# Kernel optimization log

Hardware: AMD Instinct MI355X
Metric: run time of the kernel (lower is better)

Reference implementation:

```python
import jax, jax.numpy as jnp
import numpy as np

B, N, D, NS, ITERS = 64, 4096, 256, 8, 3
EPS_ATTN = 1e-5   # module eps (added to attn)
EPS_LN = 1e-5     # torch LayerNorm default eps


def layer_norm(x, g, b):
    m = jnp.mean(x, axis=-1, keepdims=True)
    v = jnp.mean((x - m) ** 2, axis=-1, keepdims=True)
    return (x - m) / jnp.sqrt(v + EPS_LN) * g + b


def setup_inputs() -> dict:
    key = jax.random.key(0)
    ks = jax.random.split(key, 16)
    s = 0.02
    return {
        "inputs": jax.random.normal(ks[0], (B, N, D), jnp.float32),
        "slots_init": jax.random.normal(ks[1], (1, NS, D), jnp.float32),
        "Wq": jax.random.normal(ks[2], (D, D), jnp.float32) * s,
        "Wk": jax.random.normal(ks[3], (D, D), jnp.float32) * s,
        "Wv": jax.random.normal(ks[4], (D, D), jnp.float32) * s,
        "W_ih": jax.random.normal(ks[5], (3 * D, D), jnp.float32) * s,
        "W_hh": jax.random.normal(ks[6], (3 * D, D), jnp.float32) * s,
        "b_ih": jnp.zeros((3 * D,), jnp.float32),
        "b_hh": jnp.zeros((3 * D,), jnp.float32),
        "ln_in_g": jnp.ones((D,), jnp.float32),
        "ln_in_b": jnp.zeros((D,), jnp.float32),
        "ln_s_g": jnp.ones((D,), jnp.float32),
        "ln_s_b": jnp.zeros((D,), jnp.float32),
        "ln_m_g": jnp.ones((D,), jnp.float32),
        "ln_m_b": jnp.zeros((D,), jnp.float32),
        "W1": jax.random.normal(ks[7], (4 * D, D), jnp.float32) * s,
        "b1": jnp.zeros((4 * D,), jnp.float32),
        "W2": jax.random.normal(ks[8], (D, 4 * D), jnp.float32) * s,
        "b2": jnp.zeros((D,), jnp.float32),
    }


def gru_cell(x, h, W_ih, W_hh, b_ih, b_hh):
    # x, h: [M, D]; PyTorch GRU cell equations (gate order r, z, n)
    gi = x @ W_ih.T + b_ih
    gh = h @ W_hh.T + b_hh
    gi_r, gi_z, gi_n = jnp.split(gi, 3, axis=-1)
    gh_r, gh_z, gh_n = jnp.split(gh, 3, axis=-1)
    r = jax.nn.sigmoid(gi_r + gh_r)
    z = jax.nn.sigmoid(gi_z + gh_z)
    n = jnp.tanh(gi_n + r * gh_n)
    return (1.0 - z) * n + z * h


def reference(inputs, slots_init, Wq, Wk, Wv, W_ih, W_hh, b_ih, b_hh,
              ln_in_g, ln_in_b, ln_s_g, ln_s_b, ln_m_g, ln_m_b,
              W1, b1, W2, b2):
    b, n, d = inputs.shape
    scale = d ** -0.5
    slots = jnp.broadcast_to(slots_init, (b, NS, d))

    x = layer_norm(inputs, ln_in_g, ln_in_b)
    k = x @ Wk.T  # [b, n, d]
    v = x @ Wv.T  # [b, n, d]

    for _ in range(ITERS):
        slots_prev = slots
        s_n = layer_norm(slots, ln_s_g, ln_s_b)
        q = s_n @ Wq.T  # [b, ns, d]
        dots = jnp.einsum('bid,bjd->bij', q, k) * scale  # [b, ns, n]
        attn = jax.nn.softmax(dots, axis=1) + EPS_ATTN   # softmax over slots
        attn = attn / jnp.mean(attn, axis=-1, keepdims=True)
        updates = jnp.einsum('bjd,bij->bid', v, attn)     # [b, ns, d]
        h = gru_cell(updates.reshape(-1, d), slots_prev.reshape(-1, d),
                     W_ih, W_hh, b_ih, b_hh)
        slots = h.reshape(b, NS, d)
        # residual MLP with pre-norm
        y = layer_norm(slots, ln_m_g, ln_m_b)
        y = jax.nn.leaky_relu(y @ W1.T + b1, negative_slope=0.01)
        slots = slots + (y @ W2.T + b2)
    return slots
```

## Files before the change

### kernel.cpp

```cpp
#include <hip/hip_runtime.h>
#include <hip/hip_fp16.h>
#include <hip/hip_bf16.h>

#define BB 64
#define NN 4096
#define DD 256
#define NSL 8
#define NITER 3

__device__ __forceinline__ float wredsum(float v){
#pragma unroll
  for(int m=32;m;m>>=1) v += __shfl_xor(v, m, 64);
  return v;
}
__device__ __forceinline__ float2 u2f2(unsigned u){ __half2 h; __builtin_memcpy(&h,&u,4); return __half22float2(h); }
__device__ __forceinline__ float sigm(float v){ return 1.0f/(1.0f+__expf(-v)); }

union U4 { uint4 u; __half2 h[4]; };

__device__ __forceinline__ void st8(float* dst, uint4 uu){
  U4 v; v.u=uu;
  float2 f0=__half22float2(v.h[0]), f1=__half22float2(v.h[1]),
         f2=__half22float2(v.h[2]), f3=__half22float2(v.h[3]);
  dst[0]=f0.x; dst[1]=f0.y; dst[2]=f1.x; dst[3]=f1.y;
  dst[4]=f2.x; dst[5]=f2.y; dst[6]=f3.x; dst[7]=f3.y;
}

__global__ __launch_bounds__(256) void kp_all(
    const float* __restrict__ Whh, const float* __restrict__ W1,
    const float* __restrict__ W2,  const float* __restrict__ sinit,
    const float* __restrict__ Wih, const float* __restrict__ Wv,
    const float* __restrict__ Wq,  const float* __restrict__ Wk,
    __half* __restrict__ Wg, __half* __restrict__ W1t, __half* __restrict__ W2t,
    float* __restrict__ slots, __half* __restrict__ M2h, float* __restrict__ zbuf){
  int bid=blockIdx.x, t=threadIdx.x;
  if(bid<1664){
    for(int idx=bid*256+t; idx<851968; idx+=1664*256){
      if(idx<196608){ int col=idx>>8, c=idx&255; Wg[(size_t)c*1536+768+col]=__float2half(Whh[idx]); }
      else if(idx<458752){ int k=idx-196608; int col=k>>8, c=k&255; W1t[(size_t)c*1024+col]=__float2half(W1[k]); }
      else if(idx<720896){ int k=idx-458752; int col=k>>10, c=k&1023; W2t[(size_t)c*256+col]=__float2half(W2[k]); }
      else { int k=idx-720896; slots[k]=sinit[k&2047]; }
    }
  } else if(bid<2432){
    int col=bid-1664;
    __shared__ float wr[256];
    wr[t]=Wih[col*256+t];
    __syncthreads();
    float acc=0.f;
#pragma unroll 8
    for(int d=0;d<256;d++) acc += wr[d]*Wv[d*256+t];
    Wg[(size_t)t*1536+col]=__float2half(acc);
  } else if(bid<2688){
    int c=bid-2432;
    float acc=0.f;
#pragma unroll 8
    for(int d=0;d<256;d++) acc += Wq[d*256+t]*Wk[d*256+c];
    M2h[(size_t)c*256+t]=__float2half(acc*0.0625f);
  } else {
    int idx=(bid-2688)*256+t;
    if(idx<394752) zbuf[idx]=0.f;
  }
}

__global__ __launch_bounds__(256) void k_ln_x(const float* __restrict__ in, const float* __restrict__ g,
                                              const float* __restrict__ bbv, __half* __restrict__ x){
  int row  = blockIdx.x*4 + (threadIdx.x>>6);
  int lane = threadIdx.x&63;
  const float4 v = ((const float4*)(in + (size_t)row*DD))[lane];
  float s  = v.x+v.y+v.z+v.w;
  float ss = v.x*v.x+v.y*v.y+v.z*v.z+v.w*v.w;
  s = wredsum(s); ss = wredsum(ss);
  float m = s*(1.0f/256.0f);
  float r = rsqrtf(ss*(1.0f/256.0f) - m*m + 1e-5f);
  float4 gv = ((const float4*)g)[lane];
  float4 bv = ((const float4*)bbv)[lane];
  float y0=(v.x-m)*r*gv.x+bv.x, y1=(v.y-m)*r*gv.y+bv.y;
  float y2=(v.z-m)*r*gv.z+bv.z, y3=(v.w-m)*r*gv.w+bv.w;
  __half2 h0=__floats2half2_rn(y0,y1), h1=__floats2half2_rn(y2,y3);
  uint2 u; __builtin_memcpy(&u.x,&h0,4); __builtin_memcpy(&u.y,&h1,4);
  ((uint2*)(x + (size_t)row*DD))[lane] = u;
}

__global__ __launch_bounds__(256) void k_pre(const float* __restrict__ slots, const float* __restrict__ g,
                                             const float* __restrict__ bbv, const __half* __restrict__ M2h,
                                             float* __restrict__ qs, __half* __restrict__ slotsh){
  int row = blockIdx.x;
  int t = threadIdx.x;
  __shared__ __align__(16) float sn[256];
  __shared__ float red[8];
  float v = slots[row*256 + t];
  slotsh[(size_t)row*256+t]=__float2half(v);
  float s = wredsum(v), ss = wredsum(v*v);
  int wid=t>>6, lane=t&63;
  if(lane==0){ red[wid]=s; red[4+wid]=ss; }
  __syncthreads();
  float S  = red[0]+red[1]+red[2]+red[3];
  float SS = red[4]+red[5]+red[6]+red[7];
  float m = S*(1.0f/256.0f);
  float r = rsqrtf(SS*(1.0f/256.0f) - m*m + 1e-5f);
  sn[t] = (v-m)*r*g[t]+bbv[t];
  __syncthreads();
  const uint4* w4 = (const uint4*)(M2h + (size_t)t*256);
  float acc=0.f;
#pragma unroll 4
  for(int kk=0;kk<32;kk++){
    U4 w; w.u=w4[kk];
#pragma unroll
    for(int q=0;q<4;q++){
      float2 f=__half22float2(w.h[q]);
      acc += sn[kk*8+2*q]*f.x + sn[kk*8+2*q+1]*f.y;
    }
  }
  qs[row*256+t]=acc;
}

__global__ __launch_bounds__(256) void k_att(const __half* __restrict__ x, const float* __restrict__ qs,
                                             float* __restrict__ aggF, float* __restrict__ wsumF){
  int b = blockIdx.x>>4;
  int t = threadIdx.x;
  size_t j = (size_t)blockIdx.x*256 + t;
  __shared__ __align__(16) float qt[256][8];
  __shared__ __align__(16) float wl[256][8];
  __shared__ __align__(16) float aggl[4][2048];
  __shared__ float wsl[4][8];
  const float* qb = qs + b*2048;
  for(int e=t;e<2048;e+=256) qt[e&255][e>>8]=qb[e];
  __syncthreads();
  const uint4* xr = (const uint4*)(x + j*DD);
  float pd[8]={0,0,0,0,0,0,0,0};
#pragma unroll 2
  for(int ch=0; ch<32; ch++){
    uint4 u = xr[ch];
    float2 f0=u2f2(u.x), f1=u2f2(u.y), f2=u2f2(u.z), f3=u2f2(u.w);
    float xv[8]={f0.x,f0.y,f1.x,f1.y,f2.x,f2.y,f3.x,f3.y};
    int c0=ch*8;
#pragma unroll
    for(int cc=0;cc<8;cc++){
      const float4* qp=(const float4*)&qt[c0+cc][0];
      float4 qa=qp[0], qc=qp[1];
      float xvv=xv[cc];
      pd[0]+=qa.x*xvv; pd[1]+=qa.y*xvv; pd[2]+=qa.z*xvv; pd[3]+=qa.w*xvv;
      pd[4]+=qc.x*xvv; pd[5]+=qc.y*xvv; pd[6]+=qc.z*xvv; pd[7]+=qc.w*xvv;
    }
  }
  float mx=pd[0];
#pragma unroll
  for(int i=1;i<8;i++) mx=fmaxf(mx,pd[i]);
  float ev[8]; float ssum=0.f;
#pragma unroll
  for(int i=0;i<8;i++){ ev[i]=__expf(pd[i]-mx); ssum+=ev[i]; }
  float inv=1.0f/ssum;
#pragma unroll
  for(int i=0;i<8;i++) wl[t][i]=ev[i]*inv+1e-5f;
  __syncthreads();
  int wid=t>>6, lane=t&63;
  float acc[8][4];
#pragma unroll
  for(int i=0;i<8;i++){ acc[i][0]=0;acc[i][1]=0;acc[i][2]=0;acc[i][3]=0; }
  float ws[8]={0,0,0,0,0,0,0,0};
  for(int r=0;r<64;r++){
    int jl = wid*64 + r;
    uint2 u = ((const uint2*)(x + ((size_t)blockIdx.x*256 + jl)*DD))[lane];
    float2 f01=u2f2(u.x), f23=u2f2(u.y);
    const float4* wp=(const float4*)&wl[jl][0];
    float4 wa=wp[0], wb_=wp[1];
    float wv[8]={wa.x,wa.y,wa.z,wa.w,wb_.x,wb_.y,wb_.z,wb_.w};
    float xv[4]={f01.x,f01.y,f23.x,f23.y};
#pragma unroll
    for(int i=0;i<8;i++){
      acc[i][0]+=wv[i]*xv[0]; acc[i][1]+=wv[i]*xv[1];
      acc[i][2]+=wv[i]*xv[2]; acc[i][3]+=wv[i]*xv[3];
      ws[i]+=wv[i];
    }
  }
#pragma unroll
  for(int i=0;i<8;i++){
    float4 st={acc[i][0],acc[i][1],acc[i][2],acc[i][3]};
    *((float4*)&aggl[wid][i*256 + lane*4])=st;
  }
  if(lane==0){
#pragma unroll
    for(int i=0;i<8;i++) wsl[wid][i]=ws[i];
  }
  __syncthreads();
  float* ab = aggF + (size_t)b*2048;
  for(int e=t;e<2048;e+=256)
    atomicAdd(&ab[e], aggl[0][e]+aggl[1][e]+aggl[2][e]+aggl[3][e]);
  if(t<8) atomicAdd(&wsumF[b*8+t], wsl[0][t]+wsl[1][t]+wsl[2][t]+wsl[3][t]);
}

__global__ __launch_bounds__(256) void t_gates(const float* __restrict__ aggF,
    const float* __restrict__ wsumF,
    const __half* __restrict__ slotsh, const __half* __restrict__ Wg,
    const float* __restrict__ bih, const float* __restrict__ bhh,
    float* __restrict__ gl){
  int rt=blockIdx.x&15, ct=blockIdx.x>>4;
  int t=threadIdx.x;
  int r0=rt*32, c0=ct*64;
  __shared__ __align__(16) float Af[32][264];
  __shared__ __align__(16) float Wf[64][68];
  __shared__ float facS[32];
  if(ct<12){
    if(t<32) facS[t]=4096.0f/wsumF[r0+t];
    __syncthreads();
#pragma unroll
    for(int q=0;q<8;q++){
      int u=q*256+t;
      int row=u>>6, c4=u&63;
      float4 v=((const float4*)(aggF+(size_t)(r0+row)*256))[c4];
      float f=facS[row];
      v.x*=f; v.y*=f; v.z*=f; v.w*=f;
      *(float4*)&Af[row][c4*4]=v;
    }
  } else {
#pragma unroll
    for(int q=0;q<4;q++){
      int u=q*256+t;
      int row=u>>5, kk=u&31;
      st8(&Af[row][kk*8], ((const uint4*)(slotsh + ((size_t)(r0+row))*256))[kk]);
    }
  }
  float acc[2][4]={{0,0,0,0},{0,0,0,0}};
  int tx=t&15, ty=t>>4;
  for(int kc=0;kc<4;kc++){
    __syncthreads();
#pragma unroll
    for(int q=0;q<2;q++){
      int u=q*256+t;
      int kk=u>>3, cb=u&7;
      st8(&Wf[kk][cb*8], ((const uint4*)(Wg + (size_t)(kc*64+kk)*1536 + c0))[cb]);
    }
    __syncthreads();
#pragma unroll
    for(int k4=0;k4<16;k4++){
      float4 a0=*(const float4*)&Af[ty][kc*64+k4*4];
      float4 a1=*(const float4*)&Af[ty+16][kc*64+k4*4];
      float av0[4]={a0.x,a0.y,a0.z,a0.w};
      float av1[4]={a1.x,a1.y,a1.z,a1.w};
#pragma unroll
      for(int jj=0;jj<4;jj++){
        float4 wv=*(const float4*)&Wf[k4*4+jj][tx*4];
        acc[0][0]+=av0[jj]*wv.x; acc[0][1]+=av0[jj]*wv.y; acc[0][2]+=av0[jj]*wv.z; acc[0][3]+=av0[jj]*wv.w;
        acc[1][0]+=av1[jj]*wv.x; acc[1][1]+=av1[jj]*wv.y; acc[1][2]+=av1[jj]*wv.z; acc[1][3]+=av1[jj]*wv.w;
      }
    }
  }
  int col=c0+tx*4;
  const float* bb=(ct<12)? bih : bhh;
  int bcol=(ct<12)? col : col-768;
  float4 bv=*(const float4*)&bb[bcol];
  float4 o0={acc[0][0]+bv.x, acc[0][1]+bv.y, acc[0][2]+bv.z, acc[0][3]+bv.w};
  float4 o1={acc[1][0]+bv.x, acc[1][1]+bv.y, acc[1][2]+bv.z, acc[1][3]+bv.w};
  *(float4*)&gl[(size_t)(r0+ty)*1536+col]=o0;
  *(float4*)&gl[(size_t)(r0+ty+16)*1536+col]=o1;
}

__global__ __launch_bounds__(512) void t_gruln(const float* __restrict__ gl, const float* __restrict__ slots,
    const float* __restrict__ lm_g, const float* __restrict__ lm_b,
    float* __restrict__ hb, __half* __restrict__ ysh){
  int t=threadIdx.x;
  int r=t>>8, c=t&255; int row=blockIdx.x*2+r;
  __shared__ float redS[2][4], redQ[2][4];
  const float* gr = gl + (size_t)row*1536;
  float gir=gr[c], giz=gr[256+c], gin=gr[512+c];
  float ghr=gr[768+c], ghz=gr[1024+c], ghn=gr[1280+c];
  float hp = slots[(size_t)row*256+c];
  float rr=sigm(gir+ghr), z=sigm(giz+ghz);
  float n=tanhf(gin+rr*ghn);
  float hv=(1.0f-z)*n+z*hp;
  hb[(size_t)row*256+c]=hv;
  float s=wredsum(hv), ss=wredsum(hv*hv);
  if((t&63)==0){ redS[r][(t>>6)&3]=s; redQ[r][(t>>6)&3]=ss; }
  __syncthreads();
  float S=redS[r][0]+redS[r][1]+redS[r][2]+redS[r][3];
  float SS=redQ[r][0]+redQ[r][1]+redQ[r][2]+redQ[r][3];
  float m=S*(1.0f/256.0f);
  float rs=rsqrtf(SS*(1.0f/256.0f)-m*m+1e-5f);
  ysh[(size_t)row*256+c]=__float2half((hv-m)*rs*lm_g[c]+lm_b[c]);
}

__global__ __launch_bounds__(256) void t_mlp1(const __half* __restrict__ ysh,
    const __half* __restrict__ W1t, const float* __restrict__ b1,
    __half* __restrict__ z1h){
  int rt=blockIdx.x&15, ct=blockIdx.x>>4;
  int t=threadIdx.x;
  int r0=rt*32, c0=ct*64;
  __shared__ __align__(16) float Af[32][264];
  __shared__ __align__(16) float Wf[64][68];
#pragma unroll
  for(int q=0;q<4;q++){
    int u=q*256+t; int row=u>>5, kk=u&31;
    st8(&Af[row][kk*8], ((const uint4*)(ysh + ((size_t)(r0+row))*256))[kk]);
  }
  float acc[2][4]={{0,0,0,0},{0,0,0,0}};
  int tx=t&15, ty=t>>4;
  for(int kc=0;kc<4;kc++){
    __syncthreads();
#pragma unroll
    for(int q=0;q<2;q++){
      int u=q*256+t; int kk=u>>3, cb=u&7;
      st8(&Wf[kk][cb*8], ((const uint4*)(W1t + (size_t)(kc*64+kk)*1024 + c0))[cb]);
    }
    __syncthreads();
#pragma unroll
    for(int k4=0;k4<16;k4++){
      float4 a0=*(const float4*)&Af[ty][kc*64+k4*4];
      float4 a1=*(const float4*)&Af[ty+16][kc*64+k4*4];
      float av0[4]={a0.x,a0.y,a0.z,a0.w};
      float av1[4]={a1.x,a1.y,a1.z,a1.w};
#pragma unroll
      for(int jj=0;jj<4;jj++){
        float4 wv=*(const float4*)&Wf[k4*4+jj][tx*4];
        acc[0][0]+=av0[jj]*wv.x; acc[0][1]+=av0[jj]*wv.y; acc[0][2]+=av0[jj]*wv.z; acc[0][3]+=av0[jj]*wv.w;
        acc[1][0]+=av1[jj]*wv.x; acc[1][1]+=av1[jj]*wv.y; acc[1][2]+=av1[jj]*wv.z; acc[1][3]+=av1[jj]*wv.w;
      }
    }
  }
  int col=c0+tx*4;
  float4 bv=*(const float4*)&b1[col];
#pragma unroll
  for(int rr2=0;rr2<2;rr2++){
    float v0=acc[rr2][0]+bv.x, v1=acc[rr2][1]+bv.y, v2=acc[rr2][2]+bv.z, v3=acc[rr2][3]+bv.w;
    v0=v0>0.f?v0:0.01f*v0; v1=v1>0.f?v1:0.01f*v1;
    v2=v2>0.f?v2:0.01f*v2; v3=v3>0.f?v3:0.01f*v3;
    __half2 p0=__floats2half2_rn(v0,v1), p1=__floats2half2_rn(v2,v3);
    uint2 u2; __builtin_memcpy(&u2.x,&p0,4); __builtin_memcpy(&u2.y,&p1,4);
    *(uint2*)&z1h[(size_t)(r0+ty+rr2*16)*1024+col]=u2;
  }
}

__global__ __launch_bounds__(256) void t_mlp2p(const __half* __restrict__ z1h,
    const __half* __restrict__ W2t, float* __restrict__ pp){
  int b=blockIdx.x;
  int rt=b&15, ct=(b>>4)&3, kc=b>>6;
  int t=threadIdx.x;
  int r0=rt*32, c0=ct*64;
  __shared__ __align__(16) float Af[32][136];
  __shared__ __align__(16) float Wf[128][68];
#pragma unroll
  for(int q=0;q<2;q++){
    int u=q*256+t;
    int row=u>>4, seg=u&15;
    st8(&Af[row][seg*8], ((const uint4*)(z1h + (size_t)(r0+row)*1024 + kc*128))[seg]);
  }
#pragma unroll
  for(int q=0;q<4;q++){
    int u=q*256+t;
    int kk=u>>3, cb=u&7;
    st8(&Wf[kk][cb*8], ((const uint4*)(W2t + (size_t)(kc*128+kk)*256 + c0))[cb]);
  }
  __syncthreads();
  float acc[2][4]={{0,0,0,0},{0,0,0,0}};
  int tx=t&15, ty=t>>4;
#pragma unroll
  for(int k4=0;k4<32;k4++){
    float4 a0=*(const float4*)&Af[ty][k4*4];
    float4 a1=*(const float4*)&Af[ty+16][k4*4];
    float av0[4]={a0.x,a0.y,a0.z,a0.w};
    float av1[4]={a1.x,a1.y,a1.z,a1.w};
#pragma unroll
    for(int jj=0;jj<4;jj++){
      float4 wv=*(const float4*)&Wf[k4*4+jj][tx*4];
      acc[0][0]+=av0[jj]*wv.x; acc[0][1]+=av0[jj]*wv.y; acc[0][2]+=av0[jj]*wv.z; acc[0][3]+=av0[jj]*wv.w;
      acc[1][0]+=av1[jj]*wv.x; acc[1][1]+=av1[jj]*wv.y; acc[1][2]+=av1[jj]*wv.z; acc[1][3]+=av1[jj]*wv.w;
    }
  }
  int col=c0+tx*4;
  float4 o0={acc[0][0],acc[0][1],acc[0][2],acc[0][3]};
  float4 o1={acc[1][0],acc[1][1],acc[1][2],acc[1][3]};
  *(float4*)&pp[((size_t)kc*512 + r0+ty)*256+col]=o0;
  *(float4*)&pp[((size_t)kc*512 + r0+ty+16)*256+col]=o1;
}

__global__ __launch_bounds__(512) void t_fin(const float* __restrict__ hb, const float* __restrict__ pp,
    const float* __restrict__ b2, const float* __restrict__ ls_g, const float* __restrict__ ls_b,
    const __half* __restrict__ M2h, float* __restrict__ dst,
    __half* __restrict__ slotsh, float* __restrict__ qs, int last){
  int t=threadIdx.x;
  int r=t>>8, c=t&255; int row=blockIdx.x*2+r;
  __shared__ float ysl[2][256];
  __shared__ float redS[2][4], redQ[2][4];
  float s = hb[(size_t)row*256+c] + b2[c];
#pragma unroll
  for(int kc=0;kc<8;kc++) s += pp[((size_t)kc*512+row)*256+c];
  dst[(size_t)row*256+c]=s;
  if(last) return;
  slotsh[(size_t)row*256+c]=__float2half(s);
  float su=wredsum(s), sq=wredsum(s*s);
  if((t&63)==0){ redS[r][(t>>6)&3]=su; redQ[r][(t>>6)&3]=sq; }
  __syncthreads();
  float S=redS[r][0]+redS[r][1]+redS[r][2]+redS[r][3];
  float SS=redQ[r][0]+redQ[r][1]+redQ[r][2]+redQ[r][3];
  float m=S*(1.0f/256.0f);
  float rs=rsqrtf(SS*(1.0f/256.0f)-m*m+1e-5f);
  ysl[r][c]=(s-m)*rs*ls_g[c]+ls_b[c];
  __syncthreads();
  const uint4* m4=(const uint4*)(M2h+(size_t)c*256);
  float acc=0.f;
#pragma unroll 4
  for(int kk=0;kk<32;kk++){
    U4 w; w.u=m4[kk];
#pragma unroll
    for(int q=0;q<4;q++){
      float2 f=__half22float2(w.h[q]);
      acc += ysl[r][kk*8+2*q]*f.x + ysl[r][kk*8+2*q+1]*f.y;
    }
  }
  qs[(size_t)row*256+c]=acc;
}

extern "C" void kernel_launch(void* const* d_in, const int* in_sizes, int n_in,
                              void* d_out, int out_size, void* d_ws, size_t ws_size,
                              hipStream_t stream){
  const float* inputs=(const float*)d_in[0];
  const float* sinit =(const float*)d_in[1];
  const float* Wq =(const float*)d_in[2];
  const float* Wk =(const float*)d_in[3];
  const float* Wv =(const float*)d_in[4];
  const float* Wih=(const float*)d_in[5];
  const float* Whh=(const float*)d_in[6];
  const float* bih=(const float*)d_in[7];
  const float* bhh=(const float*)d_in[8];
  const float* lin_g=(const float*)d_in[9];
  const float* lin_b=(const float*)d_in[10];
  const float* ls_g=(const float*)d_in[11];
  const float* ls_b=(const float*)d_in[12];
  const float* lm_g=(const float*)d_in[13];
  const float* lm_b=(const float*)d_in[14];
  const float* W1=(const float*)d_in[15];
  const float* b1=(const float*)d_in[16];
  const float* W2=(const float*)d_in[17];
  const float* b2=(const float*)d_in[18];

  char* w=(char*)d_ws;
  __half* x    =(__half*)w; w += (size_t)BB*NN*DD*2;
  float* qs    =(float*)w;  w += 512*256*4;
  float* slots =(float*)w;  w += 512*256*4;
  __half* slotsh=(__half*)w; w += 512*256*2;
  __half* M2h  =(__half*)w; w += 256*256*2;
  __half* Wg   =(__half*)w; w += 256*1536*2;
  __half* W1t  =(__half*)w; w += 256*1024*2;
  __half* W2t  =(__half*)w; w += 1024*256*2;
  float* hb    =(float*)w;  w += 512*256*4;
  __half* ysh  =(__half*)w; w += 512*256*2;
  __half* z1h  =(__half*)w; w += (size_t)512*1024*2;
  float* pp    =(float*)w;  w += (size_t)8*512*256*4;
  float* gl_   =(float*)w;  w += (size_t)512*1536*4;
  float* aggZ  =(float*)w;  w += (size_t)(3*512*256 + 3*512)*4;

  float* aggF[3]; float* wsumF[3];
  for(int i=0;i<3;i++){ aggF[i]=aggZ + (size_t)i*512*256; wsumF[i]=aggZ + (size_t)3*512*256 + (size_t)i*512; }

  hipLaunchKernelGGL(kp_all, dim3(4230), dim3(256), 0, stream,
                     Whh, W1, W2, sinit, Wih, Wv, Wq, Wk,
                     Wg, W1t, W2t, slots, M2h, aggZ);
  hipLaunchKernelGGL(k_ln_x, dim3(65536),dim3(256), 0, stream, inputs, lin_g, lin_b, x);
  hipLaunchKernelGGL(k_pre,  dim3(512),  dim3(256), 0, stream, slots, ls_g, ls_b, M2h, qs, slotsh);
  for(int it=0; it<NITER; ++it){
    int last = (it==NITER-1);
    float* dst = last ? (float*)d_out : slots;
    hipLaunchKernelGGL(k_att,   dim3(1024), dim3(256), 0, stream, x, qs, aggF[it], wsumF[it]);
    hipLaunchKernelGGL(t_gates, dim3(384),  dim3(256), 0, stream, aggF[it], wsumF[it], slotsh, Wg, bih, bhh, gl_);
    hipLaunchKernelGGL(t_gruln, dim3(256),  dim3(512), 0, stream, gl_, slots, lm_g, lm_b, hb, ysh);
    hipLaunchKernelGGL(t_mlp1,  dim3(256),  dim3(256), 0, stream, ysh, W1t, b1, z1h);
    hipLaunchKernelGGL(t_mlp2p, dim3(512),  dim3(256), 0, stream, z1h, W2t, pp);
    hipLaunchKernelGGL(t_fin,   dim3(256),  dim3(512), 0, stream, hb, pp, b2, ls_g, ls_b, M2h,
                       dst, slotsh, qs, last);
  }
}
```

Baseline: 403.4 us.

## Fuse per-iteration GRU/MLP kernels into one cooperative kernel with grid syncs

Replaces five separate per-iteration launches (gates GEMM, GRU+LayerNorm, MLP1, MLP2 partial, finalize+next q) with one cooperative kernel. The phases are separated by grid.sync, and each phase loops over its virtual blocks with a grid-stride loop. The aim is to remove kernel launch gaps and tail idle time on this small, latency-bound part of the chain. In exchange it adds grid-wide barrier costs and caps the grid size by occupancy. The large shared buffer may also limit concurrency.

```diff
diff --git a/kernel.cpp b/kernel.cpp
--- a/kernel.cpp
+++ b/kernel.cpp
@@ -1,6 +1,10 @@
 #include <hip/hip_runtime.h>
 #include <hip/hip_fp16.h>
 #include <hip/hip_bf16.h>
+#include <hip/hip_cooperative_groups.h>
+
+namespace cg = cooperative_groups;
+
 
 #define BB 64
 #define NN 4096
@@ -189,52 +193,186 @@
   if(t<8) atomicAdd(&wsumF[b*8+t], wsl[0][t]+wsl[1][t]+wsl[2][t]+wsl[3][t]);
 }
 
-__global__ __launch_bounds__(256) void t_gates(const float* __restrict__ aggF,
-    const float* __restrict__ wsumF,
-    const __half* __restrict__ slotsh, const __half* __restrict__ Wg,
+__global__ __launch_bounds__(256) void t_all(
+    const float* __restrict__ aggF, const float* __restrict__ wsumF,
+    const float* __restrict__ slots_in, const __half* __restrict__ slotsh_r,
+    const __half* __restrict__ Wg,
     const float* __restrict__ bih, const float* __restrict__ bhh,
-    float* __restrict__ gl){
-  int rt=blockIdx.x&15, ct=blockIdx.x>>4;
-  int t=threadIdx.x;
-  int r0=rt*32, c0=ct*64;
-  __shared__ __align__(16) float Af[32][264];
-  __shared__ __align__(16) float Wf[64][68];
+    const float* __restrict__ lm_g, const float* __restrict__ lm_b,
+    const __half* __restrict__ W1t, const float* __restrict__ b1,
+    const __half* __restrict__ W2t, const float* __restrict__ b2,
+    const float* __restrict__ ls_g, const float* __restrict__ ls_b,
+    const __half* __restrict__ M2h,
+    float* __restrict__ gl, float* __restrict__ hb, __half* __restrict__ ysh,
+    __half* __restrict__ z1h, float* __restrict__ pp,
+    float* __restrict__ dst, __half* __restrict__ slotsh_w, float* __restrict__ qs,
+    int last){
+  cg::grid_group grid = cg::this_grid();
+  const int blk=blockIdx.x, t=threadIdx.x, G=gridDim.x;
+  const int lane=t&63, wid=t>>6;
+  __shared__ __align__(16) char smem[52224];
   __shared__ float facS[32];
-  if(ct<12){
-    if(t<32) facS[t]=4096.0f/wsumF[r0+t];
-    __syncthreads();
-#pragma unroll
-    for(int q=0;q<8;q++){
+  __shared__ float redS[4], redQ[4];
+  __shared__ __align__(16) float ysmall[256];
+
+  for(int vb=blk; vb<384; vb+=G){
+    __syncthreads();
+    int rt=vb&15, ct=vb>>4;
+    int r0=rt*32, c0=ct*64;
+    float (*Af)[264] = (float(*)[264])smem;
+    float (*Wf)[68]  = (float(*)[68])(smem + 33792);
+    if(ct<12){
+      if(t<32) facS[t]=4096.0f/wsumF[r0+t];
+      __syncthreads();
+#pragma unroll
+      for(int q=0;q<8;q++){
+        int u=q*256+t;
+        int row=u>>6, c4=u&63;
+        float4 v=((const float4*)(aggF+(size_t)(r0+row)*256))[c4];
+        float f=facS[row];
+        v.x*=f; v.y*=f; v.z*=f; v.w*=f;
+        *(float4*)&Af[row][c4*4]=v;
+      }
+    } else {
+#pragma unroll
+      for(int q=0;q<4;q++){
+        int u=q*256+t;
+        int row=u>>5, kk=u&31;
+        st8(&Af[row][kk*8], ((const uint4*)(slotsh_r + ((size_t)(r0+row))*256))[kk]);
+      }
+    }
+    float acc[2][4]={{0,0,0,0},{0,0,0,0}};
+    int tx=t&15, ty=t>>4;
+    for(int kc=0;kc<4;kc++){
+      __syncthreads();
+#pragma unroll
+      for(int q=0;q<2;q++){
+        int u=q*256+t;
+        int kk=u>>3, cb=u&7;
+        st8(&Wf[kk][cb*8], ((const uint4*)(Wg + (size_t)(kc*64+kk)*1536 + c0))[cb]);
+      }
+      __syncthreads();
+#pragma unroll
+      for(int k4=0;k4<16;k4++){
+        float4 a0=*(const float4*)&Af[ty][kc*64+k4*4];
+        float4 a1=*(const float4*)&Af[ty+16][kc*64+k4*4];
+        float av0[4]={a0.x,a0.y,a0.z,a0.w};
+        float av1[4]={a1.x,a1.y,a1.z,a1.w};
+#pragma unroll
+        for(int jj=0;jj<4;jj++){
+          float4 wv=*(const float4*)&Wf[k4*4+jj][tx*4];
+          acc[0][0]+=av0[jj]*wv.x; acc[0][1]+=av0[jj]*wv.y; acc[0][2]+=av0[jj]*wv.z; acc[0][3]+=av0[jj]*wv.w;
+          acc[1][0]+=av1[jj]*wv.x; acc[1][1]+=av1[jj]*wv.y; acc[1][2]+=av1[jj]*wv.z; acc[1][3]+=av1[jj]*wv.w;
+        }
+      }
+    }
+    int col=c0+tx*4;
+    const float* bb=(ct<12)? bih : bhh;
+    int bcol=(ct<12)? col : col-768;
+    float4 bv=*(const float4*)&bb[bcol];
+    float4 o0={acc[0][0]+bv.x, acc[0][1]+bv.y, acc[0][2]+bv.z, acc[0][3]+bv.w};
+    float4 o1={acc[1][0]+bv.x, acc[1][1]+bv.y, acc[1][2]+bv.z, acc[1][3]+bv.w};
+    *(float4*)&gl[(size_t)(r0+ty)*1536+col]=o0;
+    *(float4*)&gl[(size_t)(r0+ty+16)*1536+col]=o1;
+  }
+  grid.sync();
+
+  for(int row=blk; row<512; row+=G){
+    __syncthreads();
+    int c=t;
+    const float* gr = gl + (size_t)row*1536;
+    float gir=gr[c], giz=gr[256+c], gin=gr[512+c];
+    float ghr=gr[768+c], ghz=gr[1024+c], ghn=gr[1280+c];
+    float hp = slots_in[(size_t)row*256+c];
+    float rr=sigm(gir+ghr), z=sigm(giz+ghz);
+    float n=tanhf(gin+rr*ghn);
+    float hv=(1.0f-z)*n+z*hp;
+    hb[(size_t)row*256+c]=hv;
+    float s=wredsum(hv), ss=wredsum(hv*hv);
+    if(lane==0){ redS[wid]=s; redQ[wid]=ss; }
+    __syncthreads();
+    float S=redS[0]+redS[1]+redS[2]+redS[3];
+    float SS=redQ[0]+redQ[1]+redQ[2]+redQ[3];
+    float m=S*(1.0f/256.0f);
+    float rs=rsqrtf(SS*(1.0f/256.0f)-m*m+1e-5f);
+    ysh[(size_t)row*256+c]=__float2half((hv-m)*rs*lm_g[c]+lm_b[c]);
+  }
+  grid.sync();
+
+  for(int vb=blk; vb<256; vb+=G){
+    __syncthreads();
+    int rt=vb&15, ct=vb>>4;
+    int r0=rt*32, c0=ct*64;
+    float (*Af)[264] = (float(*)[264])smem;
+    float (*Wf)[68]  = (float(*)[68])(smem + 33792);
+#pragma unroll
+    for(int q=0;q<4;q++){
+      int u=q*256+t; int row=u>>5, kk=u&31;
+      st8(&Af[row][kk*8], ((const uint4*)(ysh + ((size_t)(r0+row))*256))[kk]);
+    }
+    float acc[2][4]={{0,0,0,0},{0,0,0,0}};
+    int tx=t&15, ty=t>>4;
+    for(int kc=0;kc<4;kc++){
+      __syncthreads();
+#pragma unroll
+      for(int q=0;q<2;q++){
+        int u=q*256+t; int kk=u>>3, cb=u&7;
+        st8(&Wf[kk][cb*8], ((const uint4*)(W1t + (size_t)(kc*64+kk)*1024 + c0))[cb]);
+      }
+      __syncthreads();
+#pragma unroll
+      for(int k4=0;k4<16;k4++){
+        float4 a0=*(const float4*)&Af[ty][kc*64+k4*4];
+        float4 a1=*(const float4*)&Af[ty+16][kc*64+k4*4];
+        float av0[4]={a0.x,a0.y,a0.z,a0.w};
+        float av1[4]={a1.x,a1.y,a1.z,a1.w};
+#pragma unroll
+        for(int jj=0;jj<4;jj++){
+          float4 wv=*(const float4*)&Wf[k4*4+jj][tx*4];
+          acc[0][0]+=av0[jj]*wv.x; acc[0][1]+=av0[jj]*wv.y; acc[0][2]+=av0[jj]*wv.z; acc[0][3]+=av0[jj]*wv.w;
+          acc[1][0]+=av1[jj]*wv.x; acc[1][1]+=av1[jj]*wv.y; acc[1][2]+=av1[jj]*wv.z; acc[1][3]+=av1[jj]*wv.w;
+        }
+      }
+    }
+    int col=c0+tx*4;
+    float4 bv=*(const float4*)&b1[col];
+#pragma unroll
+    for(int rr2=0;rr2<2;rr2++){
+      float v0=acc[rr2][0]+bv.x, v1=acc[rr2][1]+bv.y, v2=acc[rr2][2]+bv.z, v3=acc[rr2][3]+bv.w;
+      v0=v0>0.f?v0:0.01f*v0; v1=v1>0.f?v1:0.01f*v1;
+      v2=v2>0.f?v2:0.01f*v2; v3=v3>0.f?v3:0.01f*v3;
+      __half2 p0=__floats2half2_rn(v0,v1), p1=__floats2half2_rn(v2,v3);
+      uint2 u2; __builtin_memcpy(&u2.x,&p0,4); __builtin_memcpy(&u2.y,&p1,4);
+      *(uint2*)&z1h[(size_t)(r0+ty+rr2*16)*1024+col]=u2;
+    }
+  }
+  grid.sync();
+
+  for(int vb=blk; vb<512; vb+=G){
+    __syncthreads();
+    int rt=vb&15, ct=(vb>>4)&3, kc=vb>>6;
+    int r0=rt*32, c0=ct*64;
+    float (*Af)[136] = (float(*)[136])smem;
+    float (*Wf)[68]  = (float(*)[68])(smem + 17408);
+#pragma unroll
+    for(int q=0;q<2;q++){
       int u=q*256+t;
-      int row=u>>6, c4=u&63;
-      float4 v=((const float4*)(aggF+(size_t)(r0+row)*256))[c4];
-      float f=facS[row];
-      v.x*=f; v.y*=f; v.z*=f; v.w*=f;
-      *(float4*)&Af[row][c4*4]=v;
-    }
-  } else {
+      int row=u>>4, seg=u&15;
+      st8(&Af[row][seg*8], ((const uint4*)(z1h + (size_t)(r0+row)*1024 + kc*128))[seg]);
+    }
 #pragma unroll
     for(int q=0;q<4;q++){
       int u=q*256+t;
-      int row=u>>5, kk=u&31;
-      st8(&Af[row][kk*8], ((const uint4*)(slotsh + ((size_t)(r0+row))*256))[kk]);
-    }
-  }
-  float acc[2][4]={{0,0,0,0},{0,0,0,0}};
-  int tx=t&15, ty=t>>4;
-  for(int kc=0;kc<4;kc++){
-    __syncthreads();
-#pragma unroll
-    for(int q=0;q<2;q++){
-      int u=q*256+t;
       int kk=u>>3, cb=u&7;
-      st8(&Wf[kk][cb*8], ((const uint4*)(Wg + (size_t)(kc*64+kk)*1536 + c0))[cb]);
-    }
-    __syncthreads();
-#pragma unroll
-    for(int k4=0;k4<16;k4++){
-      float4 a0=*(const float4*)&Af[ty][kc*64+k4*4];
-      float4 a1=*(const float4*)&Af[ty+16][kc*64+k4*4];
+      st8(&Wf[kk][cb*8], ((const uint4*)(W2t + (size_t)(kc*128+kk)*256 + c0))[cb]);
+    }
+    __syncthreads();
+    float acc[2][4]={{0,0,0,0},{0,0,0,0}};
+    int tx=t&15, ty=t>>4;
+#pragma unroll
+    for(int k4=0;k4<32;k4++){
+      float4 a0=*(const float4*)&Af[ty][k4*4];
+      float4 a1=*(const float4*)&Af[ty+16][k4*4];
       float av0[4]={a0.x,a0.y,a0.z,a0.w};
       float av1[4]={a1.x,a1.y,a1.z,a1.w};
 #pragma unroll
@@ -244,169 +382,46 @@
         acc[1][0]+=av1[jj]*wv.x; acc[1][1]+=av1[jj]*wv.y; acc[1][2]+=av1[jj]*wv.z; acc[1][3]+=av1[jj]*wv.w;
       }
     }
-  }
-  int col=c0+tx*4;
-  const float* bb=(ct<12)? bih : bhh;
-  int bcol=(ct<12)? col : col-768;
-  float4 bv=*(const float4*)&bb[bcol];
-  float4 o0={acc[0][0]+bv.x, acc[0][1]+bv.y, acc[0][2]+bv.z, acc[0][3]+bv.w};
-  float4 o1={acc[1][0]+bv.x, acc[1][1]+bv.y, acc[1][2]+bv.z, acc[1][3]+bv.w};
-  *(float4*)&gl[(size_t)(r0+ty)*1536+col]=o0;
-  *(float4*)&gl[(size_t)(r0+ty+16)*1536+col]=o1;
-}
-
-__global__ __launch_bounds__(512) void t_gruln(const float* __restrict__ gl, const float* __restrict__ slots,
-    const float* __restrict__ lm_g, const float* __restrict__ lm_b,
-    float* __restrict__ hb, __half* __restrict__ ysh){
-  int t=threadIdx.x;
-  int r=t>>8, c=t&255; int row=blockIdx.x*2+r;
-  __shared__ float redS[2][4], redQ[2][4];
-  const float* gr = gl + (size_t)row*1536;
-  float gir=gr[c], giz=gr[256+c], gin=gr[512+c];
-  float ghr=gr[768+c], ghz=gr[1024+c], ghn=gr[1280+c];
-  float hp = slots[(size_t)row*256+c];
-  float rr=sigm(gir+ghr), z=sigm(giz+ghz);
-  float n=tanhf(gin+rr*ghn);
-  float hv=(1.0f-z)*n+z*hp;
-  hb[(size_t)row*256+c]=hv;
-  float s=wredsum(hv), ss=wredsum(hv*hv);
-  if((t&63)==0){ redS[r][(t>>6)&3]=s; redQ[r][(t>>6)&3]=ss; }
-  __syncthreads();
-  float S=redS[r][0]+redS[r][1]+redS[r][2]+redS[r][3];
-  float SS=redQ[r][0]+redQ[r][1]+redQ[r][2]+redQ[r][3];
-  float m=S*(1.0f/256.0f);
-  float rs=rsqrtf(SS*(1.0f/256.0f)-m*m+1e-5f);
-  ysh[(size_t)row*256+c]=__float2half((hv-m)*rs*lm_g[c]+lm_b[c]);
-}
-
-__global__ __launch_bounds__(256) void t_mlp1(const __half* __restrict__ ysh,
-    const __half* __restrict__ W1t, const float* __restrict__ b1,
-    __half* __restrict__ z1h){
-  int rt=blockIdx.x&15, ct=blockIdx.x>>4;
-  int t=threadIdx.x;
-  int r0=rt*32, c0=ct*64;
-  __shared__ __align__(16) float Af[32][264];
-  __shared__ __align__(16) float Wf[64][68];
-#pragma unroll
-  for(int q=0;q<4;q++){
-    int u=q*256+t; int row=u>>5, kk=u&31;
-    st8(&Af[row][kk*8], ((const uint4*)(ysh + ((size_t)(r0+row))*256))[kk]);
-  }
-  float acc[2][4]={{0,0,0,0},{0,0,0,0}};
-  int tx=t&15, ty=t>>4;
-  for(int kc=0;kc<4;kc++){
-    __syncthreads();
-#pragma unroll
-    for(int q=0;q<2;q++){
-      int u=q*256+t; int kk=u>>3, cb=u&7;
-      st8(&Wf[kk][cb*8], ((const uint4*)(W1t + (size_t)(kc*64+kk)*1024 + c0))[cb]);
-    }
-    __syncthreads();
-#pragma unroll
-    for(int k4=0;k4<16;k4++){
-      float4 a0=*(const float4*)&Af[ty][kc*64+k4*4];
-      float4 a1=*(const float4*)&Af[ty+16][kc*64+k4*4];
-      float av0[4]={a0.x,a0.y,a0.z,a0.w};
-      float av1[4]={a1.x,a1.y,a1.z,a1.w};
-#pragma unroll
-      for(int jj=0;jj<4;jj++){
-        float4 wv=*(const float4*)&Wf[k4*4+jj][tx*4];
-        acc[0][0]+=av0[jj]*wv.x; acc[0][1]+=av0[jj]*wv.y; acc[0][2]+=av0[jj]*wv.z; acc[0][3]+=av0[jj]*wv.w;
-        acc[1][0]+=av1[jj]*wv.x; acc[1][1]+=av1[jj]*wv.y; acc[1][2]+=av1[jj]*wv.z; acc[1][3]+=av1[jj]*wv.w;
-      }
-    }
-  }
-  int col=c0+tx*4;
-  float4 bv=*(const float4*)&b1[col];
-#pragma unroll
-  for(int rr2=0;rr2<2;rr2++){
-    float v0=acc[rr2][0]+bv.x, v1=acc[rr2][1]+bv.y, v2=acc[rr2][2]+bv.z, v3=acc[rr2][3]+bv.w;
-    v0=v0>0.f?v0:0.01f*v0; v1=v1>0.f?v1:0.01f*v1;
-    v2=v2>0.f?v2:0.01f*v2; v3=v3>0.f?v3:0.01f*v3;
-    __half2 p0=__floats2half2_rn(v0,v1), p1=__floats2half2_rn(v2,v3);
-    uint2 u2; __builtin_memcpy(&u2.x,&p0,4); __builtin_memcpy(&u2.y,&p1,4);
-    *(uint2*)&z1h[(size_t)(r0+ty+rr2*16)*1024+col]=u2;
-  }
-}
-
-__global__ __launch_bounds__(256) void t_mlp2p(const __half* __restrict__ z1h,
-    const __half* __restrict__ W2t, float* __restrict__ pp){
-  int b=blockIdx.x;
-  int rt=b&15, ct=(b>>4)&3, kc=b>>6;
-  int t=threadIdx.x;
-  int r0=rt*32, c0=ct*64;
-  __shared__ __align__(16) float Af[32][136];
-  __shared__ __align__(16) float Wf[128][68];
-#pragma unroll
-  for(int q=0;q<2;q++){
-    int u=q*256+t;
-    int row=u>>4, seg=u&15;
-    st8(&Af[row][seg*8], ((const uint4*)(z1h + (size_t)(r0+row)*1024 + kc*128))[seg]);
-  }
-#pragma unroll
-  for(int q=0;q<4;q++){
-    int u=q*256+t;
-    int kk=u>>3, cb=u&7;
-    st8(&Wf[kk][cb*8], ((const uint4*)(W2t + (size_t)(kc*128+kk)*256 + c0))[cb]);
-  }
-  __syncthreads();
-  float acc[2][4]={{0,0,0,0},{0,0,0,0}};
-  int tx=t&15, ty=t>>4;
-#pragma unroll
-  for(int k4=0;k4<32;k4++){
-    float4 a0=*(const float4*)&Af[ty][k4*4];
-    float4 a1=*(const float4*)&Af[ty+16][k4*4];
-    float av0[4]={a0.x,a0.y,a0.z,a0.w};
-    float av1[4]={a1.x,a1.y,a1.z,a1.w};
-#pragma unroll
-    for(int jj=0;jj<4;jj++){
-      float4 wv=*(const float4*)&Wf[k4*4+jj][tx*4];
-      acc[0][0]+=av0[jj]*wv.x; acc[0][1]+=av0[jj]*wv.y; acc[0][2]+=av0[jj]*wv.z; acc[0][3]+=av0[jj]*wv.w;
-      acc[1][0]+=av1[jj]*wv.x; acc[1][1]+=av1[jj]*wv.y; acc[1][2]+=av1[jj]*wv.z; acc[1][3]+=av1[jj]*wv.w;
-    }
-  }
-  int col=c0+tx*4;
-  float4 o0={acc[0][0],acc[0][1],acc[0][2],acc[0][3]};
-  float4 o1={acc[1][0],acc[1][1],acc[1][2],acc[1][3]};
-  *(float4*)&pp[((size_t)kc*512 + r0+ty)*256+col]=o0;
-  *(float4*)&pp[((size_t)kc*512 + r0+ty+16)*256+col]=o1;
-}
-
-__global__ __launch_bounds__(512) void t_fin(const float* __restrict__ hb, const float* __restrict__ pp,
-    const float* __restrict__ b2, const float* __restrict__ ls_g, const float* __restrict__ ls_b,
-    const __half* __restrict__ M2h, float* __restrict__ dst,
-    __half* __restrict__ slotsh, float* __restrict__ qs, int last){
-  int t=threadIdx.x;
-  int r=t>>8, c=t&255; int row=blockIdx.x*2+r;
-  __shared__ float ysl[2][256];
-  __shared__ float redS[2][4], redQ[2][4];
-  float s = hb[(size_t)row*256+c] + b2[c];
-#pragma unroll
-  for(int kc=0;kc<8;kc++) s += pp[((size_t)kc*512+row)*256+c];
-  dst[(size_t)row*256+c]=s;
-  if(last) return;
-  slotsh[(size_t)row*256+c]=__float2half(s);
-  float su=wredsum(s), sq=wredsum(s*s);
-  if((t&63)==0){ redS[r][(t>>6)&3]=su; redQ[r][(t>>6)&3]=sq; }
-  __syncthreads();
-  float S=redS[r][0]+redS[r][1]+redS[r][2]+redS[r][3];
-  float SS=redQ[r][0]+redQ[r][1]+redQ[r][2]+redQ[r][3];
-  float m=S*(1.0f/256.0f);
-  float rs=rsqrtf(SS*(1.0f/256.0f)-m*m+1e-5f);
-  ysl[r][c]=(s-m)*rs*ls_g[c]+ls_b[c];
-  __syncthreads();
-  const uint4* m4=(const uint4*)(M2h+(size_t)c*256);
-  float acc=0.f;
+    int col=c0+tx*4;
+    float4 o0={acc[0][0],acc[0][1],acc[0][2],acc[0][3]};
+    float4 o1={acc[1][0],acc[1][1],acc[1][2],acc[1][3]};
+    *(float4*)&pp[((size_t)kc*512 + r0+ty)*256+col]=o0;
+    *(float4*)&pp[((size_t)kc*512 + r0+ty+16)*256+col]=o1;
+  }
+  grid.sync();
+
+  for(int row=blk; row<512; row+=G){
+    __syncthreads();
+    int c=t;
+    float s = hb[(size_t)row*256+c] + b2[c];
+#pragma unroll
+    for(int kc=0;kc<8;kc++) s += pp[((size_t)kc*512+row)*256+c];
+    dst[(size_t)row*256+c]=s;
+    if(!last){
+      slotsh_w[(size_t)row*256+c]=__float2half(s);
+      float su=wredsum(s), sq=wredsum(s*s);
+      if(lane==0){ redS[wid]=su; redQ[wid]=sq; }
+      __syncthreads();
+      float S=redS[0]+redS[1]+redS[2]+redS[3];
+      float SS=redQ[0]+redQ[1]+redQ[2]+redQ[3];
+      float m=S*(1.0f/256.0f);
+      float rs=rsqrtf(SS*(1.0f/256.0f)-m*m+1e-5f);
+      ysmall[c]=(s-m)*rs*ls_g[c]+ls_b[c];
+      __syncthreads();
+      const uint4* m4=(const uint4*)(M2h+(size_t)c*256);
+      float acc=0.f;
 #pragma unroll 4
-  for(int kk=0;kk<32;kk++){
-    U4 w; w.u=m4[kk];
-#pragma unroll
-    for(int q=0;q<4;q++){
-      float2 f=__half22float2(w.h[q]);
-      acc += ysl[r][kk*8+2*q]*f.x + ysl[r][kk*8+2*q+1]*f.y;
-    }
-  }
-  qs[(size_t)row*256+c]=acc;
+      for(int kk=0;kk<32;kk++){
+        U4 w; w.u=m4[kk];
+#pragma unroll
+        for(int q=0;q<4;q++){
+          float2 f=__half22float2(w.h[q]);
+          acc += ysmall[kk*8+2*q]*f.x + ysmall[kk*8+2*q+1]*f.y;
+        }
+      }
+      qs[(size_t)row*256+c]=acc;
+    }
+  }
 }
 
 extern "C" void kernel_launch(void* const* d_in, const int* in_sizes, int n_in,
@@ -448,23 +463,37 @@
   float* gl_   =(float*)w;  w += (size_t)512*1536*4;
   float* aggZ  =(float*)w;  w += (size_t)(3*512*256 + 3*512)*4;
 
-  float* aggF[3]; float* wsumF[3];
-  for(int i=0;i<3;i++){ aggF[i]=aggZ + (size_t)i*512*256; wsumF[i]=aggZ + (size_t)3*512*256 + (size_t)i*512; }
+  float* aggFv[3]; float* wsumFv[3];
+  for(int i=0;i<3;i++){ aggFv[i]=aggZ + (size_t)i*512*256; wsumFv[i]=aggZ + (size_t)3*512*256 + (size_t)i*512; }
 
   hipLaunchKernelGGL(kp_all, dim3(4230), dim3(256), 0, stream,
                      Whh, W1, W2, sinit, Wih, Wv, Wq, Wk,
                      Wg, W1t, W2t, slots, M2h, aggZ);
   hipLaunchKernelGGL(k_ln_x, dim3(65536),dim3(256), 0, stream, inputs, lin_g, lin_b, x);
   hipLaunchKernelGGL(k_pre,  dim3(512),  dim3(256), 0, stream, slots, ls_g, ls_b, M2h, qs, slotsh);
+
+  int nb=0;
+  hipError_t e = hipOccupancyMaxActiveBlocksPerMultiprocessor(&nb, t_all, 256, 0);
+  if(e!=hipSuccess || nb<1) nb=1;
+  int gridN = nb*256; if(gridN>384) gridN=384;
+
   for(int it=0; it<NITER; ++it){
     int last = (it==NITER-1);
     float* dst = last ? (float*)d_out : slots;
-    hipLaunchKernelGGL(k_att,   dim3(1024), dim3(256), 0, stream, x, qs, aggF[it], wsumF[it]);
-    hipLaunchKernelGGL(t_gates, dim3(384),  dim3(256), 0, stream, aggF[it], wsumF[it], slotsh, Wg, bih, bhh, gl_);
-    hipLaunchKernelGGL(t_gruln, dim3(256),  dim3(512), 0, stream, gl_, slots, lm_g, lm_b, hb, ysh);
-    hipLaunchKernelGGL(t_mlp1,  dim3(256),  dim3(256), 0, stream, ysh, W1t, b1, z1h);
-    hipLaunchKernelGGL(t_mlp2p, dim3(512),  dim3(256), 0, stream, z1h, W2t, pp);
-    hipLaunchKernelGGL(t_fin,   dim3(256),  dim3(512), 0, stream, hb, pp, b2, ls_g, ls_b, M2h,
-                       dst, slotsh, qs, last);
-  }
-}
+    hipLaunchKernelGGL(k_att, dim3(1024), dim3(256), 0, stream, x, qs, aggFv[it], wsumFv[it]);
+    const float* aggC=aggFv[it]; const float* wsumC=wsumFv[it];
+    const float* slotsC=slots; const __half* slotshC=slotsh;
+    const __half* WgC=Wg; const __half* W1C=W1t; const __half* W2C=W2t; const __half* MC=M2h;
+    float* glP=gl_; float* hbP=hb; __half* yshP=ysh; __half* z1P=z1h; float* ppP=pp;
+    __half* slotshW=slotsh; float* qsP=qs;
+    void* args[] = {
+      (void*)&aggC, (void*)&wsumC, (void*)&slotsC, (void*)&slotshC, (void*)&WgC,
+      (void*)&bih, (void*)&bhh, (void*)&lm_g, (void*)&lm_b,
+      (void*)&W1C, (void*)&b1, (void*)&W2C, (void*)&b2,
+      (void*)&ls_g, (void*)&ls_b, (void*)&MC,
+      (void*)&glP, (void*)&hbP, (void*)&yshP, (void*)&z1P, (void*)&ppP,
+      (void*)&dst, (void*)&slotshW, (void*)&qsP, (void*)&last
+    };
+    hipLaunchCooperativeKernel((void*)t_all, dim3(gridN), dim3(256), args, 0, stream);
+  }
+}
```

Measured after the change: 836.1 us. 107% more time.
